# Kernel optimization log

Measured on AMD Instinct MI355X. Metric: run time of the kernel, lower is better.

Reference implementation:

```python
import jax, jax.numpy as jnp
import numpy as np

DMODEL = 1024
HEADS = 16
KEY_DIM = DMODEL // HEADS


def setup_inputs() -> dict:
    key = jax.random.key(0)
    k0, k1, k2, k3, k4 = jax.random.split(key, 5)
    scale = 1.0 / np.sqrt(DMODEL)
    return {
        "inputs": jax.random.normal(k0, (2, 2048, DMODEL), dtype=jnp.float32),
        "Wq": jax.random.normal(k1, (DMODEL, DMODEL), dtype=jnp.float32) * scale,
        "Wk": jax.random.normal(k2, (DMODEL, DMODEL), dtype=jnp.float32) * scale,
        "Wv": jax.random.normal(k3, (DMODEL, DMODEL), dtype=jnp.float32) * scale,
        "Wo": jax.random.normal(k4, (DMODEL, DMODEL), dtype=jnp.float32) * scale,
    }


def reference(inputs, Wq, Wk, Wv, Wo):
    B, S, _ = inputs.shape
    # nn.Linear(bias=False): y = x @ W.T ; then reshape to (B, S, H, Dh) and transpose to (B, H, S, Dh)
    def proj(W):
        return (inputs @ W.T).reshape(B, S, HEADS, KEY_DIM).transpose(0, 2, 1, 3)

    q, k, v = proj(Wq), proj(Wk), proj(Wv)
    scale = 1.0 / np.sqrt(KEY_DIM).astype(np.float32)
    score = jnp.einsum('bhsd,bhtd->bhst', q, k) * scale  # [B,H,S,S]
    attn = jax.nn.softmax(score, axis=-1)
    out = jnp.einsum('bhst,bhtd->bhsd', attn, v)  # [B,H,S,Dh]
    out = out.transpose(0, 2, 1, 3).reshape(B, S, HEADS * KEY_DIM)
    return out @ Wo.T
```

## Files before the change

kernel.cpp:

```cpp
#include <hip/hip_runtime.h>
#include <hip/hip_bf16.h>
#include <stdint.h>

typedef __attribute__((ext_vector_type(8))) short short8;
typedef __attribute__((ext_vector_type(4))) float floatx4;

#define MFMA16(a, b, c) __builtin_amdgcn_mfma_f32_16x16x32_bf16((a), (b), (c), 0, 0, 0)

static __device__ __forceinline__ uint16_t f2bf(float f) {
  union { float f; uint32_t u; } x; x.f = f;
  uint32_t r = x.u + 0x7fffu + ((x.u >> 16) & 1u);
  return (uint16_t)(r >> 16);
}

constexpr int DM = 1024, NH = 16, KD = 64, NB = 2, SQ = 2048;
constexpr int MTOT = NB * SQ;
constexpr int NT = SQ / 64;

__global__ void convert_kernel(const float* __restrict__ X,
                               const float* __restrict__ Wq, const float* __restrict__ Wk,
                               const float* __restrict__ Wv, const float* __restrict__ Wo,
                               uint16_t* __restrict__ Xb, uint16_t* __restrict__ Wqkvb,
                               uint16_t* __restrict__ Wob) {
  const int NX = MTOT * DM;
  const int NW = DM * DM;
  const int TOT8 = (NX + 4 * NW) / 8;
  for (int t = blockIdx.x * blockDim.x + threadIdx.x; t < TOT8; t += gridDim.x * blockDim.x) {
    int i = t * 8;
    const float* src; uint16_t* dst;
    if (i < NX) { src = X + i; dst = Xb + i; }
    else if (i < NX + 3 * NW) {
      int j = i - NX; dst = Wqkvb + j;
      src = (j < NW) ? (Wq + j) : (j < 2 * NW) ? (Wk + (j - NW)) : (Wv + (j - 2 * NW));
    } else {
      int j = i - NX - 3 * NW; src = Wo + j; dst = Wob + j;
    }
    float4 a = ((const float4*)src)[0];
    float4 b = ((const float4*)src)[1];
    ushort4 o0, o1;
    o0.x = f2bf(a.x); o0.y = f2bf(a.y); o0.z = f2bf(a.z); o0.w = f2bf(a.w);
    o1.x = f2bf(b.x); o1.y = f2bf(b.y); o1.z = f2bf(b.z); o1.w = f2bf(b.w);
    ((ushort4*)dst)[0] = o0;
    ((ushort4*)dst)[1] = o1;
  }
}

template <int MODE>
__global__ __launch_bounds__(256) void gemm_bt(const uint16_t* __restrict__ Aq,
                                               const uint16_t* __restrict__ Bq, int Ntiles,
                                               uint16_t* __restrict__ Qb, uint16_t* __restrict__ Kb,
                                               uint16_t* __restrict__ VTb, float* __restrict__ Out) {
  __shared__ uint16_t Al[128 * 32];
  __shared__ uint16_t Bl[128 * 32];
  const int K = 1024;
  int bid = blockIdx.x;
  int bm = bid / Ntiles, bn = bid % Ntiles;
  int brow = bm * 128, bcol = bn * 128;
  int tid = threadIdx.x;
  int w = tid >> 6, lane = tid & 63, g = lane >> 4, c16 = lane & 15;
  int wm = w >> 1, wn = w & 1;
  int rr = tid >> 2;
  int ce = (tid & 3) * 8;

  floatx4 acc[4][4] = {};

  for (int k0 = 0; k0 < K; k0 += 32) {
    __syncthreads();
#pragma unroll
    for (int c = 0; c < 2; ++c) {
      __builtin_amdgcn_global_load_lds(
          (const __attribute__((address_space(1))) void*)(Aq + (size_t)(brow + c * 64 + rr) * K + k0 + ce),
          (__attribute__((address_space(3))) void*)((char*)Al + c * 4096 + w * 1024), 16, 0, 0);
      __builtin_amdgcn_global_load_lds(
          (const __attribute__((address_space(1))) void*)(Bq + (size_t)(bcol + c * 64 + rr) * K + k0 + ce),
          (__attribute__((address_space(3))) void*)((char*)Bl + c * 4096 + w * 1024), 16, 0, 0);
    }
    __syncthreads();
    short8 af[4], bf[4];
#pragma unroll
    for (int mt = 0; mt < 4; ++mt)
      af[mt] = *(const short8*)&Al[(wm * 64 + mt * 16 + c16) * 32 + g * 8];
#pragma unroll
    for (int nt = 0; nt < 4; ++nt)
      bf[nt] = *(const short8*)&Bl[(wn * 64 + nt * 16 + c16) * 32 + g * 8];
#pragma unroll
    for (int mt = 0; mt < 4; ++mt)
#pragma unroll
      for (int nt = 0; nt < 4; ++nt)
        acc[mt][nt] = MFMA16(af[mt], bf[nt], acc[mt][nt]);
  }

#pragma unroll
  for (int mt = 0; mt < 4; ++mt) {
#pragma unroll
    for (int nt = 0; nt < 4; ++nt) {
      int n = bcol + wn * 64 + nt * 16 + c16;
#pragma unroll
      for (int r = 0; r < 4; ++r) {
        int m = brow + wm * 64 + mt * 16 + g * 4 + r;
        float v = acc[mt][nt][r];
        if (MODE == 0) {
          int proj = n >> 10;
          int hd = n & 1023;
          int h = hd >> 6, d = hd & 63;
          int b = m >> 11, s = m & 2047;
          size_t bh = (size_t)(b * NH + h);
          if (proj == 0) {
            Qb[(bh * SQ + s) * KD + d] = f2bf(v * 0.18033688011112042f);
          } else if (proj == 1) {
            int st = s >> 4, r2 = s & 15, k8 = d >> 3, j = d & 7;
            Kb[bh * (size_t)(SQ * KD) + (((size_t)(st * 8 + k8) * 16 + r2) * 8 + j)] = f2bf(v);
          } else {
            int kt = s >> 6, kvl = s & 63;
            int c = kvl >> 5, gg = (kvl >> 3) & 3, jj = kvl & 7;
            int dt = d >> 4, cc = d & 15;
            VTb[bh * (size_t)(SQ * KD) + (size_t)kt * 4096 +
                (size_t)(((((c * 4 + dt) * 4 + gg) * 16) + cc) * 8 + jj)] = f2bf(v);
          }
        } else {
          Out[(size_t)m * DM + n] = v;
        }
      }
    }
  }
}

__global__ __launch_bounds__(256, 4) void attn_kernel(const uint16_t* __restrict__ Q,
                                                      const uint16_t* __restrict__ Kt,
                                                      const uint16_t* __restrict__ Vt,
                                                      uint16_t* __restrict__ O) {
  __shared__ __attribute__((aligned(16))) uint16_t Kbuf[2][4096];
  __shared__ __attribute__((aligned(16))) uint16_t Plds[4][16][72];

  int bid = blockIdx.x;
  int bh = bid & 31, qt = bid >> 5;
  int qb = qt * 64;
  int b = bh >> 4, h = bh & 15;
  int tid = threadIdx.x, w = tid >> 6, lane = tid & 63, g = lane >> 4, c16 = lane & 15;

  const uint16_t* Qh = Q + (size_t)bh * SQ * KD;
  const uint16_t* Kh = Kt + (size_t)bh * SQ * KD;
  const uint16_t* Vh = Vt + (size_t)bh * SQ * KD;

  int qrow = qb + w * 16 + c16;
  short8 qf0 = *(const short8*)&Qh[(size_t)qrow * KD + g * 8];
  short8 qf1 = *(const short8*)&Qh[(size_t)qrow * KD + 32 + g * 8];

  float m = -1e30f, l = 0.0f;
  floatx4 accO[4] = {};

  auto stage_k = [&](int buf, int tile) {
#pragma unroll
    for (int i = 0; i < 2; ++i) {
      __builtin_amdgcn_global_load_lds(
          (const __attribute__((address_space(1))) void*)(Kh + (size_t)tile * 4096 + i * 2048 + tid * 8),
          (__attribute__((address_space(3))) void*)((char*)&Kbuf[buf][0] + i * 4096 + w * 1024),
          16, 0, 0);
    }
  };

  stage_k(0, 0);
  __syncthreads();

  for (int t = 0; t < NT; ++t) {
    int cur = t & 1;
    const char* kb = (const char*)&Kbuf[cur][0];

    short8 kf[4][2];
#pragma unroll
    for (int tt = 0; tt < 4; ++tt)
#pragma unroll
      for (int hf = 0; hf < 2; ++hf)
        kf[tt][hf] = *(const short8*)(kb + tt * 2048 + hf * 1024 + lane * 16);

    short8 vf[2][4];
    const uint16_t* vtile = Vh + (size_t)t * 4096;
#pragma unroll
    for (int c = 0; c < 2; ++c)
#pragma unroll
      for (int dt = 0; dt < 4; ++dt)
        vf[c][dt] = *(const short8*)&vtile[(c * 4 + dt) * 512 + lane * 8];

    stage_k(cur ^ 1, (t + 1 < NT) ? (t + 1) : t);

    floatx4 sacc[4] = {};
#pragma unroll
    for (int tt = 0; tt < 4; ++tt) {
      sacc[tt] = MFMA16(kf[tt][0], qf0, sacc[tt]);
      sacc[tt] = MFMA16(kf[tt][1], qf1, sacc[tt]);
    }

    float mt0 = fmaxf(fmaxf(sacc[0][0], sacc[0][1]), fmaxf(sacc[0][2], sacc[0][3]));
    float mt1 = fmaxf(fmaxf(sacc[1][0], sacc[1][1]), fmaxf(sacc[1][2], sacc[1][3]));
    float mt2 = fmaxf(fmaxf(sacc[2][0], sacc[2][1]), fmaxf(sacc[2][2], sacc[2][3]));
    float mt3 = fmaxf(fmaxf(sacc[3][0], sacc[3][1]), fmaxf(sacc[3][2], sacc[3][3]));
    float mx = fmaxf(fmaxf(mt0, mt1), fmaxf(mt2, mt3));
    mx = fmaxf(mx, __shfl_xor(mx, 16));
    mx = fmaxf(mx, __shfl_xor(mx, 32));
    float nm = fmaxf(m, mx);
    float al = exp2f(m - nm);
    m = nm;
    float ss = 0.0f;
#pragma unroll
    for (int tt = 0; tt < 4; ++tt) {
#pragma unroll
      for (int r = 0; r < 4; ++r)
        sacc[tt][r] = exp2f(sacc[tt][r] - nm);
      ss += (sacc[tt][0] + sacc[tt][1]) + (sacc[tt][2] + sacc[tt][3]);
    }
    ss += __shfl_xor(ss, 16);
    ss += __shfl_xor(ss, 32);
    l = l * al + ss;

    float av[4];
#pragma unroll
    for (int r = 0; r < 4; ++r) av[r] = __shfl(al, g * 4 + r);
#pragma unroll
    for (int dt = 0; dt < 4; ++dt)
#pragma unroll
      for (int r = 0; r < 4; ++r) accO[dt][r] *= av[r];

#pragma unroll
    for (int tt = 0; tt < 4; ++tt) {
      uint32_t w0 = (uint32_t)f2bf(sacc[tt][0]) | ((uint32_t)f2bf(sacc[tt][1]) << 16);
      uint32_t w1 = (uint32_t)f2bf(sacc[tt][2]) | ((uint32_t)f2bf(sacc[tt][3]) << 16);
      *(uint2*)&Plds[w][c16][tt * 16 + g * 4] = make_uint2(w0, w1);
    }
#pragma unroll
    for (int c = 0; c < 2; ++c) {
      short8 pa = *(const short8*)&Plds[w][c16][c * 32 + g * 8];
#pragma unroll
      for (int dt = 0; dt < 4; ++dt)
        accO[dt] = MFMA16(pa, vf[c][dt], accO[dt]);
    }

    __syncthreads();
  }

  float lv[4];
#pragma unroll
  for (int r = 0; r < 4; ++r) lv[r] = 1.0f / __shfl(l, g * 4 + r);
#pragma unroll
  for (int dt = 0; dt < 4; ++dt) {
#pragma unroll
    for (int r = 0; r < 4; ++r) {
      int s = qb + w * 16 + g * 4 + r;
      int d = dt * 16 + c16;
      O[((size_t)(b * SQ + s)) * DM + h * KD + d] = f2bf(accO[dt][r] * lv[r]);
    }
  }
}

extern "C" void kernel_launch(void* const* d_in, const int* in_sizes, int n_in,
                              void* d_out, int out_size, void* d_ws, size_t ws_size,
                              hipStream_t stream) {
  const float* X = (const float*)d_in[0];
  const float* Wq = (const float*)d_in[1];
  const float* Wk = (const float*)d_in[2];
  const float* Wv = (const float*)d_in[3];
  const float* Wo = (const float*)d_in[4];
  float* out = (float*)d_out;

  char* ws = (char*)d_ws;
  uint16_t* Xb    = (uint16_t*)(ws);
  uint16_t* Wqkvb = (uint16_t*)(ws + 8388608);
  uint16_t* Wob   = (uint16_t*)(ws + 14680064);
  uint16_t* Qb    = (uint16_t*)(ws + 16777216);
  uint16_t* Kb    = (uint16_t*)(ws + 25165824);
  uint16_t* VTb   = (uint16_t*)(ws + 33554432);
  uint16_t* Ob    = (uint16_t*)(ws + 41943040);

  hipLaunchKernelGGL(convert_kernel, dim3(1024), dim3(256), 0, stream,
                     X, Wq, Wk, Wv, Wo, Xb, Wqkvb, Wob);
  hipLaunchKernelGGL((gemm_bt<0>), dim3(32 * 24), dim3(256), 0, stream,
                     Xb, Wqkvb, 24, Qb, Kb, VTb, nullptr);
  hipLaunchKernelGGL(attn_kernel, dim3(1024), dim3(256), 0, stream,
                     Qb, Kb, VTb, Ob);
  hipLaunchKernelGGL((gemm_bt<1>), dim3(32 * 8), dim3(256), 0, stream,
                     Ob, Wob, 8, nullptr, nullptr, nullptr, out);
}
```

Measured before the change: 225.7 us.

## Keep attention P in registers, load K directly, lazy softmax rescale, swizzle GEMM grid

The attention kernel no longer uses LDS. K fragments are double-buffered in registers from global memory, and P is packed to bf16 with v_cvt_pk_bf16 and fed straight into the PV MFMA. To make that possible, the V layout written by the projection GEMM is permuted so it matches the MFMA output register layout. The running-max rescale is skipped while the new max stays within 8 (log2 units) of the old one, and the per-tile __syncthreads is gone. The GEMM block index is remapped across groups of 8 to improve cache locality, at the cost of higher register pressure in attention and bf16 rounding that is now round-to-nearest-even via hardware.

New measurement: 215.4 us. 1.05x faster.

```diff
diff --git a/kernel.cpp b/kernel.cpp
--- a/kernel.cpp
+++ b/kernel.cpp
@@ -11,6 +11,12 @@
   union { float f; uint32_t u; } x; x.f = f;
   uint32_t r = x.u + 0x7fffu + ((x.u >> 16) & 1u);
   return (uint16_t)(r >> 16);
+}
+
+static __device__ __forceinline__ uint32_t cvtpk_bf16(float lo, float hi) {
+  uint32_t r;
+  asm("v_cvt_pk_bf16_f32 %0, %1, %2" : "=v"(r) : "v"(lo), "v"(hi));
+  return r;
 }
 
 constexpr int DM = 1024, NH = 16, KD = 64, NB = 2, SQ = 2048;
@@ -53,7 +59,8 @@
   __shared__ uint16_t Al[128 * 32];
   __shared__ uint16_t Bl[128 * 32];
   const int K = 1024;
-  int bid = blockIdx.x;
+  int nwg = gridDim.x;
+  int bid = (blockIdx.x & 7) * (nwg >> 3) + (blockIdx.x >> 3);
   int bm = bid / Ntiles, bn = bid % Ntiles;
   int brow = bm * 128, bcol = bn * 128;
   int tid = threadIdx.x;
@@ -112,10 +119,11 @@
             Kb[bh * (size_t)(SQ * KD) + (((size_t)(st * 8 + k8) * 16 + r2) * 8 + j)] = f2bf(v);
           } else {
             int kt = s >> 6, kvl = s & 63;
-            int c = kvl >> 5, gg = (kvl >> 3) & 3, jj = kvl & 7;
+            int c = kvl >> 5, tth = (kvl >> 4) & 1, gg = (kvl >> 2) & 3, rs = kvl & 3;
+            int jp = tth * 4 + rs;
             int dt = d >> 4, cc = d & 15;
             VTb[bh * (size_t)(SQ * KD) + (size_t)kt * 4096 +
-                (size_t)(((((c * 4 + dt) * 4 + gg) * 16) + cc) * 8 + jj)] = f2bf(v);
+                (size_t)((c * 4 + dt) * 512 + gg * 128 + cc * 8 + jp)] = f2bf(v);
           }
         } else {
           Out[(size_t)m * DM + n] = v;
@@ -129,9 +137,6 @@
                                                       const uint16_t* __restrict__ Kt,
                                                       const uint16_t* __restrict__ Vt,
                                                       uint16_t* __restrict__ O) {
-  __shared__ __attribute__((aligned(16))) uint16_t Kbuf[2][4096];
-  __shared__ __attribute__((aligned(16))) uint16_t Plds[4][16][72];
-
   int bid = blockIdx.x;
   int bh = bid & 31, qt = bid >> 5;
   int qb = qt * 64;
@@ -149,29 +154,20 @@
   float m = -1e30f, l = 0.0f;
   floatx4 accO[4] = {};
 
-  auto stage_k = [&](int buf, int tile) {
-#pragma unroll
-    for (int i = 0; i < 2; ++i) {
-      __builtin_amdgcn_global_load_lds(
-          (const __attribute__((address_space(1))) void*)(Kh + (size_t)tile * 4096 + i * 2048 + tid * 8),
-          (__attribute__((address_space(3))) void*)((char*)&Kbuf[buf][0] + i * 4096 + w * 1024),
-          16, 0, 0);
-    }
-  };
-
-  stage_k(0, 0);
-  __syncthreads();
-
+  short8 kfb[2][4][2];
+#define LOADK(buf, tile)                                                              \
+  {                                                                                   \
+    const uint16_t* kt_ = Kh + (size_t)(tile) * 4096;                                 \
+    _Pragma("unroll") for (int tt = 0; tt < 4; ++tt)                                  \
+        _Pragma("unroll") for (int hf = 0; hf < 2; ++hf)                              \
+            kfb[buf][tt][hf] = *(const short8*)&kt_[tt * 1024 + hf * 512 + lane * 8]; \
+  }
+
+  LOADK(0, 0);
+
+#pragma unroll 2
   for (int t = 0; t < NT; ++t) {
     int cur = t & 1;
-    const char* kb = (const char*)&Kbuf[cur][0];
-
-    short8 kf[4][2];
-#pragma unroll
-    for (int tt = 0; tt < 4; ++tt)
-#pragma unroll
-      for (int hf = 0; hf < 2; ++hf)
-        kf[tt][hf] = *(const short8*)(kb + tt * 2048 + hf * 1024 + lane * 16);
 
     short8 vf[2][4];
     const uint16_t* vtile = Vh + (size_t)t * 4096;
@@ -181,61 +177,61 @@
       for (int dt = 0; dt < 4; ++dt)
         vf[c][dt] = *(const short8*)&vtile[(c * 4 + dt) * 512 + lane * 8];
 
-    stage_k(cur ^ 1, (t + 1 < NT) ? (t + 1) : t);
-
     floatx4 sacc[4] = {};
 #pragma unroll
     for (int tt = 0; tt < 4; ++tt) {
-      sacc[tt] = MFMA16(kf[tt][0], qf0, sacc[tt]);
-      sacc[tt] = MFMA16(kf[tt][1], qf1, sacc[tt]);
-    }
-
-    float mt0 = fmaxf(fmaxf(sacc[0][0], sacc[0][1]), fmaxf(sacc[0][2], sacc[0][3]));
-    float mt1 = fmaxf(fmaxf(sacc[1][0], sacc[1][1]), fmaxf(sacc[1][2], sacc[1][3]));
-    float mt2 = fmaxf(fmaxf(sacc[2][0], sacc[2][1]), fmaxf(sacc[2][2], sacc[2][3]));
-    float mt3 = fmaxf(fmaxf(sacc[3][0], sacc[3][1]), fmaxf(sacc[3][2], sacc[3][3]));
-    float mx = fmaxf(fmaxf(mt0, mt1), fmaxf(mt2, mt3));
+      sacc[tt] = MFMA16(kfb[cur][tt][0], qf0, sacc[tt]);
+      sacc[tt] = MFMA16(kfb[cur][tt][1], qf1, sacc[tt]);
+    }
+
+    LOADK(cur ^ 1, (t + 1 < NT) ? (t + 1) : t);
+
+    float mx = fmaxf(fmaxf(fmaxf(sacc[0][0], sacc[0][1]), fmaxf(sacc[0][2], sacc[0][3])),
+                     fmaxf(fmaxf(sacc[1][0], sacc[1][1]), fmaxf(sacc[1][2], sacc[1][3])));
+    mx = fmaxf(mx, fmaxf(fmaxf(fmaxf(sacc[2][0], sacc[2][1]), fmaxf(sacc[2][2], sacc[2][3])),
+                         fmaxf(fmaxf(sacc[3][0], sacc[3][1]), fmaxf(sacc[3][2], sacc[3][3]))));
     mx = fmaxf(mx, __shfl_xor(mx, 16));
     mx = fmaxf(mx, __shfl_xor(mx, 32));
-    float nm = fmaxf(m, mx);
-    float al = exp2f(m - nm);
-    m = nm;
+    if (!__all(mx <= m + 8.0f)) {
+      float nm = fmaxf(m, mx);
+      float al = exp2f(m - nm);
+      m = nm;
+      l *= al;
+      float av[4];
+#pragma unroll
+      for (int r = 0; r < 4; ++r) av[r] = __shfl(al, g * 4 + r);
+#pragma unroll
+      for (int dt = 0; dt < 4; ++dt)
+#pragma unroll
+        for (int r = 0; r < 4; ++r) accO[dt][r] *= av[r];
+    }
     float ss = 0.0f;
 #pragma unroll
     for (int tt = 0; tt < 4; ++tt) {
 #pragma unroll
       for (int r = 0; r < 4; ++r)
-        sacc[tt][r] = exp2f(sacc[tt][r] - nm);
+        sacc[tt][r] = exp2f(sacc[tt][r] - m);
       ss += (sacc[tt][0] + sacc[tt][1]) + (sacc[tt][2] + sacc[tt][3]);
     }
     ss += __shfl_xor(ss, 16);
     ss += __shfl_xor(ss, 32);
-    l = l * al + ss;
-
-    float av[4];
-#pragma unroll
-    for (int r = 0; r < 4; ++r) av[r] = __shfl(al, g * 4 + r);
-#pragma unroll
-    for (int dt = 0; dt < 4; ++dt)
-#pragma unroll
-      for (int r = 0; r < 4; ++r) accO[dt][r] *= av[r];
-
-#pragma unroll
-    for (int tt = 0; tt < 4; ++tt) {
-      uint32_t w0 = (uint32_t)f2bf(sacc[tt][0]) | ((uint32_t)f2bf(sacc[tt][1]) << 16);
-      uint32_t w1 = (uint32_t)f2bf(sacc[tt][2]) | ((uint32_t)f2bf(sacc[tt][3]) << 16);
-      *(uint2*)&Plds[w][c16][tt * 16 + g * 4] = make_uint2(w0, w1);
-    }
+    l += ss;
+
+    union { uint32_t u[4]; short8 s8; } pa[2];
 #pragma unroll
     for (int c = 0; c < 2; ++c) {
-      short8 pa = *(const short8*)&Plds[w][c16][c * 32 + g * 8];
+      pa[c].u[0] = cvtpk_bf16(sacc[2 * c][0], sacc[2 * c][1]);
+      pa[c].u[1] = cvtpk_bf16(sacc[2 * c][2], sacc[2 * c][3]);
+      pa[c].u[2] = cvtpk_bf16(sacc[2 * c + 1][0], sacc[2 * c + 1][1]);
+      pa[c].u[3] = cvtpk_bf16(sacc[2 * c + 1][2], sacc[2 * c + 1][3]);
+    }
+#pragma unroll
+    for (int c = 0; c < 2; ++c)
 #pragma unroll
       for (int dt = 0; dt < 4; ++dt)
-        accO[dt] = MFMA16(pa, vf[c][dt], accO[dt]);
-    }
-
-    __syncthreads();
-  }
+        accO[dt] = MFMA16(pa[c].s8, vf[c][dt], accO[dt]);
+  }
+#undef LOADK
 
   float lv[4];
 #pragma unroll
```
